# Performance work log

Measured on AMD Instinct MI355X. Metric: run time of the kernel, lower is better.

## Reference

```python
import jax, jax.numpy as jnp
import numpy as np

MIN_RET = 0.1
TCI = 0.99
LN_EPS = 1e-6
BN_EPS = 1e-3


def _ln(x, g, b):
    m = x.mean(-1, keepdims=True)
    v = x.var(-1, keepdims=True)
    return (x - m) * jax.lax.rsqrt(v + LN_EPS) * g + b


def _mha(x, wq, bq, wk, bk, wv, bv, wo, bo):
    # keras MultiHeadAttention, inference (dropout off). Returns (out, weights[B,H,Tq,Tk]).
    dk = wq.shape[-1]
    q = jnp.einsum('bsd,dhk->bshk', x, wq) + bq
    k = jnp.einsum('bsd,dhk->bshk', x, wk) + bk
    v = jnp.einsum('bsd,dhk->bshk', x, wv) + bv
    s = jnp.einsum('bqhk,bshk->bhqs', q, k) * (1.0 / np.sqrt(dk))
    w = jax.nn.softmax(s, axis=-1)
    o = jnp.einsum('bhqs,bshk->bqhk', w, v)
    return jnp.einsum('bqhk,hkd->bqd', o, wo) + bo, w


def _trunk(x, ln1_g, ln1_b, ln2_g, ln2_b, ln3_g, ln3_b,
           gq_w, gq_b, gk_w, gk_b, gv_w, gv_b, go_w, go_b,
           lq_w, lq_b, lk_w, lk_b, lv_w, lv_b, lo_w, lo_b,
           ffn_w1, ffn_b1, ffn_w2, ffn_b2):
    norm1 = _ln(x, ln1_g, ln1_b)
    a, aw = _mha(norm1, gq_w, gq_b, gk_w, gk_b, gv_w, gv_b, go_w, go_b)
    out1 = x + a
    norm2 = _ln(out1, ln2_g, ln2_b)
    la, law = _mha(norm2, lq_w, lq_b, lk_w, lk_b, lv_w, lv_b, lo_w, lo_b)
    out2 = out1 + la
    norm3 = _ln(out2, ln3_g, ln3_b)
    f = jnp.maximum(norm3 @ ffn_w1 + ffn_b1, 0.0) @ ffn_w2 + ffn_b2
    return out2 + f, aw, law


def _topk_indices(aw, law, seq_len):
    # importance: mean over heads then over query dim -> [B, Tk]
    imp = 0.7 * aw.mean(axis=(1, 2)) + 0.3 * law.mean(axis=(1, 2))
    imp = imp / (imp.sum(-1, keepdims=True) + 1e-10)
    sv, si = jax.lax.top_k(imp, imp.shape[-1])
    cum = jnp.cumsum(sv, axis=-1)
    num = (cum <= TCI).sum(-1)
    min_pts = int(round(seq_len * MIN_RET))
    num = jnp.minimum(jnp.maximum(num, min_pts), seq_len)
    # padded-to-common-k version of the per-sample ragged stack in the original
    k = int(jnp.max(num))
    return jnp.sort(si[:, :k], axis=-1)


def reference(x, ln1_g, ln1_b, ln2_g, ln2_b, ln3_g, ln3_b,
              gq_w, gq_b, gk_w, gk_b, gv_w, gv_b, go_w, go_b,
              lq_w, lq_b, lk_w, lk_b, lv_w, lv_b, lo_w, lo_b,
              ffn_w1, ffn_b1, ffn_w2, ffn_b2,
              res_w, res_b, bn_g, bn_b, bn_mean, bn_var):
    out3, aw, law = _trunk(x, ln1_g, ln1_b, ln2_g, ln2_b, ln3_g, ln3_b,
                           gq_w, gq_b, gk_w, gk_b, gv_w, gv_b, go_w, go_b,
                           lq_w, lq_b, lk_w, lk_b, lv_w, lv_b, lo_w, lo_b,
                           ffn_w1, ffn_b1, ffn_w2, ffn_b2)
    idx = _topk_indices(aw, law, x.shape[1])  # [B, K]
    gather = lambda t: jnp.take_along_axis(t, idx[..., None], axis=1)
    down = gather(out3) + gather(x @ res_w + res_b)
    # BatchNorm, inference mode (moving stats)
    down = (down - bn_mean) * jax.lax.rsqrt(bn_var + BN_EPS) * bn_g + bn_b
    return down, idx


def setup_inputs() -> dict:
    B, S, D, H, F = 4, 2048, 256, 8, 1024
    dk = D // H
    ks = iter(jax.random.split(jax.random.key(0), 32))
    w = lambda *sh: jax.random.normal(next(ks), sh, jnp.float32) * 0.02
    inp = {'x': jax.random.normal(next(ks), (B, S, D), jnp.float32)}
    for nm in ('ln1', 'ln2', 'ln3'):
        inp[nm + '_g'] = jnp.ones((D,), jnp.float32)
        inp[nm + '_b'] = jnp.zeros((D,), jnp.float32)
    for p in ('g', 'l'):
        for t in ('q', 'k', 'v'):
            inp[f'{p}{t}_w'] = w(D, H, dk)
            inp[f'{p}{t}_b'] = jnp.zeros((H, dk), jnp.float32)
        inp[f'{p}o_w'] = w(H, dk, D)
        inp[f'{p}o_b'] = jnp.zeros((D,), jnp.float32)
    inp['ffn_w1'] = w(D, F); inp['ffn_b1'] = jnp.zeros((F,), jnp.float32)
    inp['ffn_w2'] = w(F, D); inp['ffn_b2'] = jnp.zeros((D,), jnp.float32)
    inp['res_w'] = w(D, D); inp['res_b'] = jnp.zeros((D,), jnp.float32)
    inp['bn_g'] = jnp.ones((D,), jnp.float32)
    inp['bn_b'] = jnp.zeros((D,), jnp.float32)
    inp['bn_mean'] = jnp.zeros((D,), jnp.float32)
    inp['bn_var'] = jnp.ones((D,), jnp.float32)
    return inp
```

## Files before the change

### kernel.cpp

```cpp
#include <hip/hip_runtime.h>

#define SEQ 2048
#define DM 256
#define NH 8
#define DKH 32
#define NBATCH 4
#define QSCALE (0.17677669529663687f * 1.4426950408889634f)

#if __has_builtin(__builtin_amdgcn_exp2f)
#define EXP2(x) __builtin_amdgcn_exp2f(x)
#else
#define EXP2(x) exp2f(x)
#endif

typedef __attribute__((ext_vector_type(8))) __bf16 bf16x8;
typedef __attribute__((ext_vector_type(4))) float floatx4;
typedef __attribute__((ext_vector_type(8))) short short8v;
typedef __attribute__((ext_vector_type(2))) unsigned int uint2v;

__device__ inline unsigned short f2bf(float x){
  union { float f; unsigned u; } v; v.f = x;
  unsigned r = v.u + 0x7FFFu + ((v.u >> 16) & 1u);
  return (unsigned short)(r >> 16);
}
__device__ inline unsigned pack2bf(float a, float b){
  union { float f; unsigned u; } ua, ub; ua.f = a; ub.f = b;
  return __builtin_amdgcn_perm(ub.u, ua.u, 0x07060302u);
}

__global__ __launch_bounds__(256) void ln_kernel(const float* __restrict__ X,
    const float* __restrict__ G, const float* __restrict__ Bv,
    unsigned short* __restrict__ Y){
  int row = blockIdx.x*4 + (threadIdx.x>>6);
  int lane = threadIdx.x & 63;
  const float4 v = *(const float4*)(X + (size_t)row*DM + lane*4);
  float s = v.x+v.y+v.z+v.w;
  #pragma unroll
  for (int off=32; off; off>>=1) s += __shfl_xor(s, off, 64);
  float mean = s * (1.0f/DM);
  float dx=v.x-mean, dy=v.y-mean, dz=v.z-mean, dw=v.w-mean;
  float ss = dx*dx+dy*dy+dz*dz+dw*dw;
  #pragma unroll
  for (int off=32; off; off>>=1) ss += __shfl_xor(ss, off, 64);
  float r = rsqrtf(ss*(1.0f/DM) + 1e-6f);
  const float4 g = *(const float4*)(G + lane*4);
  const float4 b = *(const float4*)(Bv + lane*4);
  ushort4 o;
  o.x = f2bf(dx*r*g.x + b.x);
  o.y = f2bf(dy*r*g.y + b.y);
  o.z = f2bf(dz*r*g.z + b.z);
  o.w = f2bf(dw*r*g.w + b.w);
  *(ushort4*)(Y + (size_t)row*DM + lane*4) = o;
}

struct WtArgs {
  const float* src[12];
  unsigned short* dst[12];
  int K[12], N[12], stride[12], off[12];
  int blk0[13];
};
__global__ __launch_bounds__(256) void wtrans_all(WtArgs a){
  __shared__ unsigned short sT[64][40];
  int wi = 0;
  while (blockIdx.x >= (unsigned)a.blk0[wi+1]) ++wi;
  int blk = blockIdx.x - a.blk0[wi];
  int tid = threadIdx.x;
  if (wi == 11){
    const float* X = a.src[11];
    unsigned short* D = a.dst[11];
    int row = blk*8 + (tid>>5);
    int c8 = (tid & 31)*8;
    const float* ip = X + (size_t)row*256 + c8;
    float4 v0 = *(const float4*)ip, v1 = *(const float4*)(ip+4);
    union { short8v v; unsigned short u[8]; } pk;
    pk.u[0]=f2bf(v0.x); pk.u[1]=f2bf(v0.y); pk.u[2]=f2bf(v0.z); pk.u[3]=f2bf(v0.w);
    pk.u[4]=f2bf(v1.x); pk.u[5]=f2bf(v1.y); pk.u[6]=f2bf(v1.z); pk.u[7]=f2bf(v1.w);
    *(short8v*)(D + (size_t)row*1280 + 1024 + c8) = pk.v;
    return;
  }
  const float* W = a.src[wi];
  unsigned short* Wt = a.dst[wi];
  int K = a.K[wi], N = a.N[wi], stride = a.stride[wi], off = a.off[wi];
  int nbk = N >> 6;
  int bx = blk % nbk, by = blk / nbk;
  int k0 = by << 5, n0 = bx << 6;
  int r = tid >> 3, cs = (tid & 7) << 3;
  const float* ip = W + (size_t)(k0+r)*N + n0 + cs;
  float4 av = *(const float4*)ip;
  float4 bq = *(const float4*)(ip+4);
  sT[cs+0][r]=f2bf(av.x); sT[cs+1][r]=f2bf(av.y); sT[cs+2][r]=f2bf(av.z); sT[cs+3][r]=f2bf(av.w);
  sT[cs+4][r]=f2bf(bq.x); sT[cs+5][r]=f2bf(bq.y); sT[cs+6][r]=f2bf(bq.z); sT[cs+7][r]=f2bf(bq.w);
  __syncthreads();
  int n = tid >> 2, kc = (tid & 3) << 3;
  *(short8v*)(Wt + (size_t)(n0+n)*stride + off + k0 + kc) = *(const short8v*)(&sT[n][kc]);
}

__global__ __launch_bounds__(256) void gemm_bf16(const unsigned short* __restrict__ A,
    const unsigned short* __restrict__ Bt, const float* __restrict__ bias,
    const float* __restrict__ Res, void* __restrict__ Cout,
    int M, int N, int K, int flags, float outscale, int ldc){
  __shared__ unsigned short sA[8192];
  __shared__ unsigned short sB[4096];
  int nbk = N >> 6;
  int bx = blockIdx.x % nbk, by = blockIdx.x / nbk;
  int m0 = by << 7, n0 = bx << 6;
  int tid = threadIdx.x, w = tid >> 6, lane = tid & 63;
  int m16 = lane & 15, quad = lane >> 4;
  int wr = w & 1, wc = w >> 1;
  const unsigned short* pa[4]; const unsigned short* pb[2];
  #pragma unroll
  for (int i=0;i<4;++i){
    int c = tid + i*256;
    int l = c & 63, kk = (c>>6)&1, mt = c>>7;
    pa[i] = A + (size_t)(m0 + mt*16 + (l&15))*K + kk*32 + ((l>>4)<<3);
  }
  #pragma unroll
  for (int i=0;i<2;++i){
    int c = tid + i*256;
    int l = c & 63, kk = (c>>6)&1, nt = c>>7;
    pb[i] = Bt + (size_t)(n0 + nt*16 + (l&15))*K + kk*32 + ((l>>4)<<3);
  }
  short8v ar[4], br[2];
  #pragma unroll
  for (int i=0;i<4;++i) ar[i] = *(const short8v*)pa[i];
  #pragma unroll
  for (int i=0;i<2;++i) br[i] = *(const short8v*)pb[i];
  floatx4 acc[4][2];
  #pragma unroll
  for (int i=0;i<4;++i){ acc[i][0]=(floatx4){0,0,0,0}; acc[i][1]=(floatx4){0,0,0,0}; }
  for (int k0=0; k0<K; k0+=64){
    __syncthreads();
    #pragma unroll
    for (int i=0;i<4;++i) *(short8v*)(sA + (tid+i*256)*8) = ar[i];
    #pragma unroll
    for (int i=0;i<2;++i) *(short8v*)(sB + (tid+i*256)*8) = br[i];
    __syncthreads();
    if (k0 + 64 < K){
      #pragma unroll
      for (int i=0;i<4;++i) ar[i] = *(const short8v*)(pa[i] + k0 + 64);
      #pragma unroll
      for (int i=0;i<2;++i) br[i] = *(const short8v*)(pb[i] + k0 + 64);
    }
    #pragma unroll
    for (int kk=0;kk<2;++kk){
      bf16x8 bf0 = *(const bf16x8*)(sB + (((wc*2+0)*2+kk)*64 + lane)*8);
      bf16x8 bf1 = *(const bf16x8*)(sB + (((wc*2+1)*2+kk)*64 + lane)*8);
      #pragma unroll
      for (int mt=0;mt<4;++mt){
        bf16x8 af = *(const bf16x8*)(sA + (((wr*4+mt)*2+kk)*64 + lane)*8);
        acc[mt][0] = __builtin_amdgcn_mfma_f32_16x16x32_bf16(af, bf0, acc[mt][0], 0,0,0);
        acc[mt][1] = __builtin_amdgcn_mfma_f32_16x16x32_bf16(af, bf1, acc[mt][1], 0,0,0);
      }
    }
  }
  float b0 = bias ? bias[n0 + wc*32 + m16]      : 0.0f;
  float b1 = bias ? bias[n0 + wc*32 + 16 + m16] : 0.0f;
  #pragma unroll
  for (int mt=0;mt<4;++mt){
    #pragma unroll
    for (int r=0;r<4;++r){
      size_t row = (size_t)m0 + wr*64 + mt*16 + quad*4 + r;
      int col0 = n0 + wc*32 + m16, col1 = col0 + 16;
      float v0 = acc[mt][0][r] + b0, v1 = acc[mt][1][r] + b1;
      if (Res){ v0 += Res[row*N + col0]; v1 += Res[row*N + col1]; }
      if (flags & 1){ v0 = fmaxf(v0, 0.0f); v1 = fmaxf(v1, 0.0f); }
      v0 *= outscale; v1 *= outscale;
      if (flags & 2){
        unsigned short* C = (unsigned short*)Cout;
        C[row*ldc + col0] = f2bf(v0); C[row*ldc + col1] = f2bf(v1);
      } else {
        float* C = (float*)Cout;
        C[row*ldc + col0] = v0; C[row*ldc + col1] = v1;
      }
    }
  }
}

__global__ __launch_bounds__(256) void gemm64(const unsigned short* __restrict__ A,
    const unsigned short* __restrict__ Bt, const float* __restrict__ bias,
    const float* __restrict__ bias2, const float* __restrict__ Res,
    void* __restrict__ Cout, int M, int N, int K, int flags, float outscale){
  __shared__ unsigned short sA[4096];
  __shared__ unsigned short sB[4096];
  int nbk = N >> 6;
  int bx = blockIdx.x % nbk, by = blockIdx.x / nbk;
  int m0 = by << 6, n0 = bx << 6;
  int tid = threadIdx.x, w = tid >> 6, lane = tid & 63;
  int m16 = lane & 15, quad = lane >> 4;
  int wr = w & 1, wc = w >> 1;
  const unsigned short* pa[2]; const unsigned short* pb[2];
  #pragma unroll
  for (int i=0;i<2;++i){
    int c = tid + i*256;
    int l = c & 63, kk = (c>>6)&1, mt = c>>7;
    int col = kk*32 + ((l>>4)<<3);
    pa[i] = A  + (size_t)(m0 + mt*16 + (l&15))*K + col;
    pb[i] = Bt + (size_t)(n0 + mt*16 + (l&15))*K + col;
  }
  short8v ar[2], br[2];
  #pragma unroll
  for (int i=0;i<2;++i){ ar[i] = *(const short8v*)pa[i]; br[i] = *(const short8v*)pb[i]; }
  floatx4 acc[2][2];
  acc[0][0]=(floatx4){0,0,0,0}; acc[0][1]=(floatx4){0,0,0,0};
  acc[1][0]=(floatx4){0,0,0,0}; acc[1][1]=(floatx4){0,0,0,0};
  for (int k0=0; k0<K; k0+=64){
    __syncthreads();
    #pragma unroll
    for (int i=0;i<2;++i){
      *(short8v*)(sA + (tid+i*256)*8) = ar[i];
      *(short8v*)(sB + (tid+i*256)*8) = br[i];
    }
    __syncthreads();
    if (k0 + 64 < K){
      #pragma unroll
      for (int i=0;i<2;++i){ ar[i] = *(const short8v*)(pa[i]+k0+64); br[i] = *(const short8v*)(pb[i]+k0+64); }
    }
    #pragma unroll
    for (int kk=0;kk<2;++kk){
      bf16x8 bf0 = *(const bf16x8*)(sB + (((wc*2+0)*2+kk)*64 + lane)*8);
      bf16x8 bf1 = *(const bf16x8*)(sB + (((wc*2+1)*2+kk)*64 + lane)*8);
      bf16x8 af0 = *(const bf16x8*)(sA + (((wr*2+0)*2+kk)*64 + lane)*8);
      bf16x8 af1 = *(const bf16x8*)(sA + (((wr*2+1)*2+kk)*64 + lane)*8);
      acc[0][0] = __builtin_amdgcn_mfma_f32_16x16x32_bf16(af0, bf0, acc[0][0], 0,0,0);
      acc[0][1] = __builtin_amdgcn_mfma_f32_16x16x32_bf16(af0, bf1, acc[0][1], 0,0,0);
      acc[1][0] = __builtin_amdgcn_mfma_f32_16x16x32_bf16(af1, bf0, acc[1][0], 0,0,0);
      acc[1][1] = __builtin_amdgcn_mfma_f32_16x16x32_bf16(af1, bf1, acc[1][1], 0,0,0);
    }
  }
  float b0 = bias ? bias[n0 + wc*32 + m16]      : 0.0f;
  float b1 = bias ? bias[n0 + wc*32 + 16 + m16] : 0.0f;
  if (bias2){ b0 += bias2[n0 + wc*32 + m16]; b1 += bias2[n0 + wc*32 + 16 + m16]; }
  #pragma unroll
  for (int mt=0;mt<2;++mt){
    #pragma unroll
    for (int r=0;r<4;++r){
      size_t row = (size_t)m0 + (wr*2+mt)*16 + quad*4 + r;
      int col0 = n0 + wc*32 + m16, col1 = col0 + 16;
      float v0 = acc[mt][0][r] + b0, v1 = acc[mt][1][r] + b1;
      if (Res){ v0 += Res[row*N + col0]; v1 += Res[row*N + col1]; }
      if (flags & 1){ v0 = fmaxf(v0, 0.0f); v1 = fmaxf(v1, 0.0f); }
      v0 *= outscale; v1 *= outscale;
      if (flags & 2){
        unsigned short* C = (unsigned short*)Cout;
        C[row*N + col0] = f2bf(v0); C[row*N + col1] = f2bf(v1);
      } else {
        float* C = (float*)Cout;
        C[row*N + col0] = v0; C[row*N + col1] = v1;
      }
    }
  }
}

__global__ __launch_bounds__(256) void gemm_qkv(const unsigned short* __restrict__ A,
    const unsigned short* __restrict__ Bt,
    const float* __restrict__ bq, const float* __restrict__ bk, const float* __restrict__ bv,
    unsigned short* __restrict__ outq, unsigned short* __restrict__ outk,
    unsigned short* __restrict__ outvt){
  __shared__ unsigned short sA[8192];
  __shared__ unsigned short sB[4096];
  int bx = blockIdx.x % 12, by = blockIdx.x / 12;
  int m0 = by << 7, n0 = bx << 6;
  int tid = threadIdx.x, w = tid >> 6, lane = tid & 63;
  int m16 = lane & 15, quad = lane >> 4;
  int wr = w & 1, wc = w >> 1;
  const unsigned short* pa[4]; const unsigned short* pb[2];
  #pragma unroll
  for (int i=0;i<4;++i){
    int c = tid + i*256;
    int l = c & 63, kk = (c>>6)&1, mt = c>>7;
    pa[i] = A + (size_t)(m0 + mt*16 + (l&15))*256 + kk*32 + ((l>>4)<<3);
  }
  #pragma unroll
  for (int i=0;i<2;++i){
    int c = tid + i*256;
    int l = c & 63, kk = (c>>6)&1, nt = c>>7;
    pb[i] = Bt + (size_t)(n0 + nt*16 + (l&15))*256 + kk*32 + ((l>>4)<<3);
  }
  short8v ar[4], br[2];
  #pragma unroll
  for (int i=0;i<4;++i) ar[i] = *(const short8v*)pa[i];
  #pragma unroll
  for (int i=0;i<2;++i) br[i] = *(const short8v*)pb[i];
  floatx4 acc[4][2];
  #pragma unroll
  for (int i=0;i<4;++i){ acc[i][0]=(floatx4){0,0,0,0}; acc[i][1]=(floatx4){0,0,0,0}; }
  for (int k0=0; k0<256; k0+=64){
    __syncthreads();
    #pragma unroll
    for (int i=0;i<4;++i) *(short8v*)(sA + (tid+i*256)*8) = ar[i];
    #pragma unroll
    for (int i=0;i<2;++i) *(short8v*)(sB + (tid+i*256)*8) = br[i];
    __syncthreads();
    if (k0 + 64 < 256){
      #pragma unroll
      for (int i=0;i<4;++i) ar[i] = *(const short8v*)(pa[i] + k0 + 64);
      #pragma unroll
      for (int i=0;i<2;++i) br[i] = *(const short8v*)(pb[i] + k0 + 64);
    }
    #pragma unroll
    for (int kk=0;kk<2;++kk){
      bf16x8 bf0 = *(const bf16x8*)(sB + (((wc*2+0)*2+kk)*64 + lane)*8);
      bf16x8 bf1 = *(const bf16x8*)(sB + (((wc*2+1)*2+kk)*64 + lane)*8);
      #pragma unroll
      for (int mt=0;mt<4;++mt){
        bf16x8 af = *(const bf16x8*)(sA + (((wr*4+mt)*2+kk)*64 + lane)*8);
        acc[mt][0] = __builtin_amdgcn_mfma_f32_16x16x32_bf16(af, bf0, acc[mt][0], 0,0,0);
        acc[mt][1] = __builtin_amdgcn_mfma_f32_16x16x32_bf16(af, bf1, acc[mt][1], 0,0,0);
      }
    }
  }
  int seg = n0 >> 8;
  int nb  = n0 & 255;
  const float* bias = (seg==0) ? bq : ((seg==1) ? bk : bv);
  float b0 = bias[nb + wc*32 + m16];
  float b1 = bias[nb + wc*32 + 16 + m16];
  if (seg == 2){
    int b = m0 >> 11;
    int t0 = (m0 & 2047) + wr*64 + quad*4;
    #pragma unroll
    for (int mt=0;mt<4;++mt){
      int t = t0 + mt*16;
      #pragma unroll
      for (int cc=0;cc<2;++cc){
        int col = nb + wc*32 + m16 + cc*16;
        float bb = cc ? b1 : b0;
        int hh = col >> 5, dd = col & 31;
        uint2v pk;
        pk.x = (unsigned)f2bf(acc[mt][cc][0]+bb) | ((unsigned)f2bf(acc[mt][cc][1]+bb) << 16);
        pk.y = (unsigned)f2bf(acc[mt][cc][2]+bb) | ((unsigned)f2bf(acc[mt][cc][3]+bb) << 16);
        *(uint2v*)(outvt + ((size_t)((b*8+hh)*32+dd))*SEQ + t) = pk;
      }
    }
  } else {
    unsigned short* C = (seg==0) ? outq : outk;
    float scale = (seg==0) ? QSCALE : 1.0f;
    #pragma unroll
    for (int mt=0;mt<4;++mt){
      #pragma unroll
      for (int r=0;r<4;++r){
        size_t row = (size_t)m0 + wr*64 + mt*16 + quad*4 + r;
        int col0 = nb + wc*32 + m16, col1 = col0 + 16;
        C[row*256 + col0] = f2bf((acc[mt][0][r] + b0)*scale);
        C[row*256 + col1] = f2bf((acc[mt][1][r] + b1)*scale);
      }
    }
  }
}

__global__ __launch_bounds__(256) void flash_kernel(
    const unsigned short* __restrict__ Qb, const unsigned short* __restrict__ Kb,
    const unsigned short* __restrict__ Vt, unsigned short* __restrict__ Obf,
    float* __restrict__ Lout){
  __shared__ unsigned short sK[4096];
  __shared__ unsigned short sV[4096];
  __shared__ unsigned short sP[4*16*136];
  int qb = blockIdx.x & 31, bh = blockIdx.x >> 5;
  int h = bh & 7, b = bh >> 3;
  int tid = threadIdx.x, w = tid >> 6, lane = tid & 63;
  int m16 = lane & 15, quad = lane >> 4;
  int qrow0 = qb*64 + w*16;
  bf16x8 qf = *(const bf16x8*)(Qb + (size_t)(b*SEQ + qrow0 + m16)*DM + h*DKH + quad*8);
  floatx4 o0 = {0,0,0,0}, o1 = {0,0,0,0};
  float l0 = 0.f;
  unsigned short* sPw = sP + w*2176;

  const unsigned short* kp[2]; const unsigned short* vp[2];
  #pragma unroll
  for (int i=0;i<2;++i){
    int c = tid + i*256, l = c & 63;
    int kt = c >> 6;
    kp[i] = Kb + (size_t)(b*SEQ + kt*16 + (l&15))*DM + h*DKH + ((l>>4)<<3);
    int nt = (c>>6)&1, ks = c>>7;
    vp[i] = Vt + (size_t)(bh*DKH + nt*16 + (l&15))*SEQ + ks*32 + ((l>>4)<<3);
  }
  short8v kr[2], vr[2];
  #pragma unroll
  for (int i=0;i<2;++i){ kr[i] = *(const short8v*)kp[i]; vr[i] = *(const short8v*)vp[i]; }

  for (int t0=0; t0<SEQ; t0+=128){
    __syncthreads();
    #pragma unroll
    for (int i=0;i<2;++i){
      *(short8v*)(sK + (tid+i*256)*8) = kr[i];
      *(short8v*)(sV + (tid+i*256)*8) = vr[i];
    }
    __syncthreads();
    if (t0 + 128 < SEQ){
      #pragma unroll
      for (int i=0;i<2;++i){
        kr[i] = *(const short8v*)(kp[i] + (size_t)(t0+128)*DM);
        vr[i] = *(const short8v*)(vp[i] + (t0+128));
      }
    }
    #pragma unroll
    for (int kt=0;kt<8;++kt){
      bf16x8 kf = *(const bf16x8*)(sK + (kt*64+lane)*8);
      floatx4 z = {0,0,0,0};
      floatx4 s = __builtin_amdgcn_mfma_f32_16x16x32_bf16(kf, qf, z, 0,0,0);
      float p0 = EXP2(s[0]), p1 = EXP2(s[1]), p2 = EXP2(s[2]), p3 = EXP2(s[3]);
      l0 += (p0+p1)+(p2+p3);
      uint2v pk; pk.x = pack2bf(p0,p1); pk.y = pack2bf(p2,p3);
      *(uint2v*)(sPw + m16*136 + kt*16 + quad*4) = pk;
    }
    #pragma unroll
    for (int ks=0;ks<4;++ks){
      bf16x8 pf  = *(const bf16x8*)(sPw + m16*136 + ks*32 + quad*8);
      bf16x8 vf0 = *(const bf16x8*)(sV + ((ks*2+0)*64+lane)*8);
      bf16x8 vf1 = *(const bf16x8*)(sV + ((ks*2+1)*64+lane)*8);
      o0 = __builtin_amdgcn_mfma_f32_16x16x32_bf16(pf, vf0, o0, 0,0,0);
      o1 = __builtin_amdgcn_mfma_f32_16x16x32_bf16(pf, vf1, o1, 0,0,0);
    }
  }
  l0 += __shfl_xor(l0, 16, 64);
  l0 += __shfl_xor(l0, 32, 64);
  float inv = 1.0f / l0;
  #pragma unroll
  for (int r=0;r<4;++r){
    float iv = __shfl(inv, quad*4 + r, 64);
    int q = qrow0 + quad*4 + r;
    size_t base = (size_t)(b*SEQ + q)*DM + h*DKH;
    Obf[base + m16]      = f2bf(o0[r]*iv);
    Obf[base + 16 + m16] = f2bf(o1[r]*iv);
    if (m16 == 0) Lout[(size_t)bh*SEQ + q] = iv;
  }
}

__global__ __launch_bounds__(128) void colsum_kernel(
    const unsigned short* __restrict__ Qb, const unsigned short* __restrict__ Kb,
    const float* __restrict__ Lv, float* __restrict__ col){
  __shared__ unsigned short sQ[2048];
  __shared__ float sL[64];
  int kc = blockIdx.x & 31;
  int rest = blockIdx.x >> 5;
  int bh = rest & 31;
  int half = rest >> 5;
  int h = bh & 7, b = bh >> 3;
  int tid = threadIdx.x, w = tid >> 6, lane = tid & 63;
  int m16 = lane & 15, quad = lane >> 4;
  int key0 = kc*64 + w*32;
  const unsigned short* kp = Kb + (size_t)(b*SEQ + key0 + m16)*DM + h*DKH + quad*8;
  bf16x8 kf0 = *(const bf16x8*)kp;
  bf16x8 kf1 = *(const bf16x8*)(kp + 16*DM);
  float acc0[4] = {0,0,0,0}, acc1[4] = {0,0,0,0};
  const unsigned short* qp[2];
  #pragma unroll
  for (int i=0;i<2;++i){
    int c = tid + i*128, l = c & 63, qt = c >> 6;
    qp[i] = Qb + (size_t)(b*SEQ + half*1024 + qt*16 + (l&15))*DM + h*DKH + ((l>>4)<<3);
  }
  short8v qr[2];
  #pragma unroll
  for (int i=0;i<2;++i) qr[i] = *(const short8v*)qp[i];
  float lr = (tid < 64) ? Lv[(size_t)bh*SEQ + half*1024 + tid] : 0.0f;
  for (int q0=0; q0<1024; q0+=64){
    __syncthreads();
    #pragma unroll
    for (int i=0;i<2;++i) *(short8v*)(sQ + (tid+i*128)*8) = qr[i];
    if (tid < 64) sL[tid] = lr;
    __syncthreads();
    if (q0 + 64 < 1024){
      #pragma unroll
      for (int i=0;i<2;++i) qr[i] = *(const short8v*)(qp[i] + (size_t)(q0+64)*DM);
      if (tid < 64) lr = Lv[(size_t)bh*SEQ + half*1024 + q0 + 64 + tid];
    }
    floatx4 z = {0,0,0,0};
    #pragma unroll
    for (int qt2=0;qt2<4;++qt2){
      bf16x8 qf = *(const bf16x8*)(sQ + (qt2*64+lane)*8);
      floatx4 t0 = __builtin_amdgcn_mfma_f32_16x16x32_bf16(kf0, qf, z, 0,0,0);
      floatx4 t1 = __builtin_amdgcn_mfma_f32_16x16x32_bf16(kf1, qf, z, 0,0,0);
      float lq = sL[qt2*16+m16];
      #pragma unroll
      for (int r=0;r<4;++r){ acc0[r] += EXP2(t0[r])*lq; acc1[r] += EXP2(t1[r])*lq; }
    }
  }
  #pragma unroll
  for (int r=0;r<4;++r){
    float v0 = acc0[r], v1 = acc1[r];
    v0 += __shfl_xor(v0, 1, 64); v0 += __shfl_xor(v0, 2, 64);
    v0 += __shfl_xor(v0, 4, 64); v0 += __shfl_xor(v0, 8, 64);
    v1 += __shfl_xor(v1, 1, 64); v1 += __shfl_xor(v1, 2, 64);
    v1 += __shfl_xor(v1, 4, 64); v1 += __shfl_xor(v1, 8, 64);
    if (m16 == 0){
      size_t base = (size_t)(half*32 + bh)*SEQ;
      col[base + key0 + quad*4 + r]      = v0;
      col[base + key0 + 16 + quad*4 + r] = v1;
    }
  }
}

__global__ __launch_bounds__(128) void imp_kernel(const float* __restrict__ colG,
    const float* __restrict__ colL, float* __restrict__ imp){
  int i = blockIdx.x*128 + threadIdx.x;
  int b = i >> 11, t = i & 2047;
  double sg = 0.0, sl = 0.0;
  for (int h=0; h<8; ++h){
    size_t i0 = (size_t)(b*8+h)*SEQ + t;
    size_t i1 = (size_t)(32 + b*8+h)*SEQ + t;
    sg += (double)colG[i0] + (double)colG[i1];
    sl += (double)colL[i0] + (double)colL[i1];
  }
  imp[i] = (float)(0.7*sg + 0.3*sl);
}

__global__ __launch_bounds__(256) void rank_part(const float* __restrict__ imp,
    int* __restrict__ rp){
  __shared__ float sj[256];
  int jc = blockIdx.x & 7;
  int ic = (blockIdx.x >> 3) & 7;
  int b  = blockIdx.x >> 6;
  int tid = threadIdx.x;
  sj[tid] = imp[b*2048 + jc*256 + tid];
  __syncthreads();
  int i = ic*256 + tid;
  float v = imp[b*2048 + i];
  int jbase = jc*256;
  int r = 0;
  #pragma unroll 4
  for (int j=0; j<256; j+=4){
    float4 vj = *(const float4*)&sj[j];
    r += (vj.x > v) || (vj.x == v && (jbase+j+0) < i);
    r += (vj.y > v) || (vj.y == v && (jbase+j+1) < i);
    r += (vj.z > v) || (vj.z == v && (jbase+j+2) < i);
    r += (vj.w > v) || (vj.w == v && (jbase+j+3) < i);
  }
  rp[(size_t)jc*8192 + b*2048 + i] = r;
}

__global__ __launch_bounds__(256) void compact_kernel(const int* __restrict__ rp,
    int KK, int* __restrict__ idxout){
  __shared__ int swave[4];
  int b = blockIdx.x;
  int tid = threadIdx.x, w = tid >> 6, lane = tid & 63;
  int base = tid*8;
  int f[8]; int c = 0;
  #pragma unroll
  for (int j=0;j<8;++j){
    int rr = 0;
    #pragma unroll
    for (int c2=0;c2<8;++c2) rr += rp[(size_t)c2*8192 + b*2048 + base + j];
    f[j] = (rr < KK) ? 1 : 0; c += f[j];
  }
  int pref = c;
  #pragma unroll
  for (int off=1; off<64; off<<=1){
    int t = __shfl_up(pref, off, 64);
    if (lane >= off) pref += t;
  }
  if (lane == 63) swave[w] = pref;
  __syncthreads();
  int wbase = 0;
  for (int k=0;k<w;++k) wbase += swave[k];
  int pos = wbase + pref - c;
  #pragma unroll
  for (int j=0;j<8;++j){
    if (f[j]) idxout[b*KK + pos++] = base + j;
  }
}

__global__ __launch_bounds__(256) void final_kernel(const float* __restrict__ rb,
    const int* __restrict__ idx, const float* __restrict__ g, const float* __restrict__ bt,
    const float* __restrict__ mean, const float* __restrict__ var,
    float* __restrict__ out, int KK){
  int row = blockIdx.x*4 + (threadIdx.x>>6);
  int lane = threadIdx.x & 63;
  int total = NBATCH*KK;
  if (row < total){
    int b = row / KK;
    int src = idx[row];
    float4 v  = *(const float4*)(rb + ((size_t)(b*SEQ+src))*DM + lane*4);
    float4 gm = *(const float4*)(mean + lane*4);
    float4 gv = *(const float4*)(var  + lane*4);
    float4 gg = *(const float4*)(g    + lane*4);
    float4 gb = *(const float4*)(bt   + lane*4);
    float4 o;
    o.x = (v.x-gm.x)*rsqrtf(gv.x+1e-3f)*gg.x + gb.x;
    o.y = (v.y-gm.y)*rsqrtf(gv.y+1e-3f)*gg.y + gb.y;
    o.z = (v.z-gm.z)*rsqrtf(gv.z+1e-3f)*gg.z + gb.z;
    o.w = (v.w-gm.w)*rsqrtf(gv.w+1e-3f)*gg.w + gb.w;
    *(float4*)(out + (size_t)row*DM + lane*4) = o;
  }
  int gid = blockIdx.x*256 + threadIdx.x;
  if (gid < total) out[(size_t)total*DM + gid] = (float)idx[gid];
}

extern "C" void kernel_launch(void* const* d_in, const int* in_sizes, int n_in,
                              void* d_out, int out_size, void* d_ws, size_t ws_size,
                              hipStream_t stream){
  (void)in_sizes; (void)n_in; (void)ws_size;
  const float* x    = (const float*)d_in[0];
  const float* ln1g = (const float*)d_in[1];
  const float* ln1b = (const float*)d_in[2];
  const float* ln2g = (const float*)d_in[3];
  const float* ln2b = (const float*)d_in[4];
  const float* ln3g = (const float*)d_in[5];
  const float* ln3b = (const float*)d_in[6];
  const float* gqw = (const float*)d_in[7];  const float* gqb = (const float*)d_in[8];
  const float* gkw = (const float*)d_in[9];  const float* gkb = (const float*)d_in[10];
  const float* gvw = (const float*)d_in[11]; const float* gvb = (const float*)d_in[12];
  const float* gow = (const float*)d_in[13]; const float* gob = (const float*)d_in[14];
  const float* lqw = (const float*)d_in[15]; const float* lqb = (const float*)d_in[16];
  const float* lkw = (const float*)d_in[17]; const float* lkb = (const float*)d_in[18];
  const float* lvw = (const float*)d_in[19]; const float* lvb = (const float*)d_in[20];
  const float* low = (const float*)d_in[21]; const float* lob = (const float*)d_in[22];
  const float* fw1 = (const float*)d_in[23]; const float* fb1 = (const float*)d_in[24];
  const float* fw2 = (const float*)d_in[25]; const float* fb2 = (const float*)d_in[26];
  const float* resw = (const float*)d_in[27]; const float* resb = (const float*)d_in[28];
  const float* bng = (const float*)d_in[29]; const float* bnb = (const float*)d_in[30];
  const float* bnm = (const float*)d_in[31]; const float* bnv = (const float*)d_in[32];

  float* ws = (float*)d_ws;
  const size_t M1 = 2097152;
  float* r1 = ws;
  float* r2 = ws + M1;
  float* r3 = ws + 2*M1;
  unsigned short* nb  = (unsigned short*)(ws + 3*M1);
  unsigned short* qbf = (unsigned short*)(ws + 3*M1 + M1/2);
  unsigned short* kbf = (unsigned short*)(ws + 4*M1);
  unsigned short* vtb = (unsigned short*)(ws + 4*M1 + M1/2);
  unsigned short* obf = (unsigned short*)(ws + 5*M1);
  unsigned short* Acat = (unsigned short*)(ws + 6*M1);
  unsigned short* wT  = (unsigned short*)(ws + 9*M1);
  unsigned short* wgq = wT;            unsigned short* wgk = wT + 65536;
  unsigned short* wgv = wT + 131072;   unsigned short* wgo = wT + 196608;
  unsigned short* wlq = wT + 262144;   unsigned short* wlk = wT + 327680;
  unsigned short* wlv = wT + 393216;   unsigned short* wlo = wT + 458752;
  unsigned short* wf1  = wT + 524288;
  unsigned short* wcat = wT + 786432;
  float* Ls   = ws + 10*M1;
  float* colG = ws + 10*M1 + 65536;
  float* colL = ws + 10*M1 + 196608;
  float* impb = ws + 10*M1 + 327680;
  int*   rpb  = (int*)(ws + 10*M1 + 335872);
  int*   idxb = (int*)(ws + 10*M1 + 401408);

  int KK = out_size / (NBATCH*(DM+1));
  float* out = (float*)d_out;

  WtArgs wa;
  const float* srcs[12] = {gqw,gkw,gvw,gow,lqw,lkw,lvw,low, fw1, fw2, resw, x};
  unsigned short* dsts[12] = {wgq,wgk,wgv,wgo,wlq,wlk,wlv,wlo, wf1, wcat, wcat, Acat};
  int Ks[12]  = {256,256,256,256,256,256,256,256, 256, 1024, 256, 0};
  int Ns[12]  = {256,256,256,256,256,256,256,256, 1024, 256, 256, 0};
  int Ss[12]  = {256,256,256,256,256,256,256,256, 256, 1280, 1280, 0};
  int Os[12]  = {0,0,0,0,0,0,0,0, 0, 0, 1024, 0};
  int acc = 0;
  for (int i=0;i<12;++i){
    wa.src[i]=srcs[i]; wa.dst[i]=dsts[i]; wa.K[i]=Ks[i]; wa.N[i]=Ns[i];
    wa.stride[i]=Ss[i]; wa.off[i]=Os[i];
    wa.blk0[i]=acc;
    acc += (i==11) ? 1024 : (Ks[i]>>5)*(Ns[i]>>6);
  }
  wa.blk0[12]=acc;
  wtrans_all<<<acc,256,0,stream>>>(wa);

  ln_kernel<<<2048,256,0,stream>>>(x, ln1g, ln1b, nb);
  gemm_qkv<<<768,256,0,stream>>>(nb, wgq, gqb, gkb, gvb, qbf, kbf, vtb);
  flash_kernel<<<1024,256,0,stream>>>(qbf, kbf, vtb, obf, Ls);
  colsum_kernel<<<2048,128,0,stream>>>(qbf, kbf, Ls, colG);
  gemm64<<<512,256,0,stream>>>(obf, wgo, gob, nullptr, x, r1, 8192,256,256, 0, 1.0f);

  ln_kernel<<<2048,256,0,stream>>>(r1, ln2g, ln2b, nb);
  gemm_qkv<<<768,256,0,stream>>>(nb, wlq, lqb, lkb, lvb, qbf, kbf, vtb);
  flash_kernel<<<1024,256,0,stream>>>(qbf, kbf, vtb, obf, Ls);
  colsum_kernel<<<2048,128,0,stream>>>(qbf, kbf, Ls, colL);
  gemm64<<<512,256,0,stream>>>(obf, wlo, lob, nullptr, r1, r2, 8192,256,256, 0, 1.0f);

  ln_kernel<<<2048,256,0,stream>>>(r2, ln3g, ln3b, nb);
  gemm_bf16<<<1024,256,0,stream>>>(nb, wf1, fb1, nullptr, Acat, 8192,1024,256, 1|2, 1.0f, 1280);
  gemm64<<<512,256,0,stream>>>(Acat, wcat, fb2, resb, r2, r3, 8192,256,1280, 0, 1.0f);

  imp_kernel<<<64,128,0,stream>>>(colG, colL, impb);
  rank_part<<<256,256,0,stream>>>(impb, rpb);
  compact_kernel<<<NBATCH,256,0,stream>>>(rpb, KK, idxb);
  int total = NBATCH*KK;
  final_kernel<<<(total+3)/4,256,0,stream>>>(r3, idxb, bng, bnb, bnm, bnv, out, KK);
}
```

Measured before the change: 361.5 us.

## Split flash attention over key halves and keep P in registers

Attention is now split across two key-range halves, doubling the block count. Each half writes unnormalized fp32 partial outputs and row sums, and a new reduce kernel combines them, normalizes, and writes the bf16 output and inverse sums. The V-transpose store now uses a permuted token order so the exponentiated scores can feed the PV MFMA straight from registers, which removes the per-wave shared-memory P buffer. In exchange it adds an extra kernel launch and an fp32 partial round-trip through global memory, and it raises the launch-bounds occupancy hint.

Measured after the change: 390.9 us. 8.1% more time.

```diff
diff --git a/kernel.cpp b/kernel.cpp
--- a/kernel.cpp
+++ b/kernel.cpp
@@ -319,7 +319,8 @@
     int t0 = (m0 & 2047) + wr*64 + quad*4;
     #pragma unroll
     for (int mt=0;mt<4;++mt){
-      int t = t0 + mt*16;
+      int tt = t0 + mt*16;
+      int tp = (tt & ~31) | (((tt>>2)&3)<<3) | (((tt>>4)&1)<<2);
       #pragma unroll
       for (int cc=0;cc<2;++cc){
         int col = nb + wc*32 + m16 + cc*16;
@@ -328,7 +329,7 @@
         uint2v pk;
         pk.x = (unsigned)f2bf(acc[mt][cc][0]+bb) | ((unsigned)f2bf(acc[mt][cc][1]+bb) << 16);
         pk.y = (unsigned)f2bf(acc[mt][cc][2]+bb) | ((unsigned)f2bf(acc[mt][cc][3]+bb) << 16);
-        *(uint2v*)(outvt + ((size_t)((b*8+hh)*32+dd))*SEQ + t) = pk;
+        *(uint2v*)(outvt + ((size_t)((b*8+hh)*32+dd))*SEQ + tp) = pk;
       }
     }
   } else {
@@ -347,14 +348,15 @@
   }
 }
 
-__global__ __launch_bounds__(256) void flash_kernel(
+__global__ __launch_bounds__(256, 8) void flash_kernel(
     const unsigned short* __restrict__ Qb, const unsigned short* __restrict__ Kb,
-    const unsigned short* __restrict__ Vt, unsigned short* __restrict__ Obf,
-    float* __restrict__ Lout){
+    const unsigned short* __restrict__ Vt, float* __restrict__ opart,
+    float* __restrict__ lpart){
   __shared__ unsigned short sK[4096];
   __shared__ unsigned short sV[4096];
-  __shared__ unsigned short sP[4*16*136];
-  int qb = blockIdx.x & 31, bh = blockIdx.x >> 5;
+  int qb = blockIdx.x & 31;
+  int bh = (blockIdx.x >> 5) & 31;
+  int half = blockIdx.x >> 10;
   int h = bh & 7, b = bh >> 3;
   int tid = threadIdx.x, w = tid >> 6, lane = tid & 63;
   int m16 = lane & 15, quad = lane >> 4;
@@ -362,7 +364,7 @@
   bf16x8 qf = *(const bf16x8*)(Qb + (size_t)(b*SEQ + qrow0 + m16)*DM + h*DKH + quad*8);
   floatx4 o0 = {0,0,0,0}, o1 = {0,0,0,0};
   float l0 = 0.f;
-  unsigned short* sPw = sP + w*2176;
+  int tbeg = half*1024;
 
   const unsigned short* kp[2]; const unsigned short* vp[2];
   #pragma unroll
@@ -375,9 +377,12 @@
   }
   short8v kr[2], vr[2];
   #pragma unroll
-  for (int i=0;i<2;++i){ kr[i] = *(const short8v*)kp[i]; vr[i] = *(const short8v*)vp[i]; }
-
-  for (int t0=0; t0<SEQ; t0+=128){
+  for (int i=0;i<2;++i){
+    kr[i] = *(const short8v*)(kp[i] + (size_t)tbeg*DM);
+    vr[i] = *(const short8v*)(vp[i] + tbeg);
+  }
+
+  for (int t0=tbeg; t0<tbeg+1024; t0+=128){
     __syncthreads();
     #pragma unroll
     for (int i=0;i<2;++i){
@@ -385,7 +390,7 @@
       *(short8v*)(sV + (tid+i*256)*8) = vr[i];
     }
     __syncthreads();
-    if (t0 + 128 < SEQ){
+    if (t0 + 128 < tbeg + 1024){
       #pragma unroll
       for (int i=0;i<2;++i){
         kr[i] = *(const short8v*)(kp[i] + (size_t)(t0+128)*DM);
@@ -393,36 +398,55 @@
       }
     }
     #pragma unroll
-    for (int kt=0;kt<8;++kt){
-      bf16x8 kf = *(const bf16x8*)(sK + (kt*64+lane)*8);
+    for (int ks=0;ks<4;++ks){
+      bf16x8 kf0 = *(const bf16x8*)(sK + ((ks*2+0)*64+lane)*8);
+      bf16x8 kf1 = *(const bf16x8*)(sK + ((ks*2+1)*64+lane)*8);
       floatx4 z = {0,0,0,0};
-      floatx4 s = __builtin_amdgcn_mfma_f32_16x16x32_bf16(kf, qf, z, 0,0,0);
-      float p0 = EXP2(s[0]), p1 = EXP2(s[1]), p2 = EXP2(s[2]), p3 = EXP2(s[3]);
-      l0 += (p0+p1)+(p2+p3);
-      uint2v pk; pk.x = pack2bf(p0,p1); pk.y = pack2bf(p2,p3);
-      *(uint2v*)(sPw + m16*136 + kt*16 + quad*4) = pk;
-    }
-    #pragma unroll
-    for (int ks=0;ks<4;++ks){
-      bf16x8 pf  = *(const bf16x8*)(sPw + m16*136 + ks*32 + quad*8);
+      floatx4 s0 = __builtin_amdgcn_mfma_f32_16x16x32_bf16(kf0, qf, z, 0,0,0);
+      floatx4 s1 = __builtin_amdgcn_mfma_f32_16x16x32_bf16(kf1, qf, z, 0,0,0);
+      float p0 = EXP2(s0[0]), p1 = EXP2(s0[1]), p2 = EXP2(s0[2]), p3 = EXP2(s0[3]);
+      float p4 = EXP2(s1[0]), p5 = EXP2(s1[1]), p6 = EXP2(s1[2]), p7 = EXP2(s1[3]);
+      l0 += ((p0+p1)+(p2+p3)) + ((p4+p5)+(p6+p7));
+      union { bf16x8 v; unsigned u[4]; } pf;
+      pf.u[0] = pack2bf(p0,p1); pf.u[1] = pack2bf(p2,p3);
+      pf.u[2] = pack2bf(p4,p5); pf.u[3] = pack2bf(p6,p7);
       bf16x8 vf0 = *(const bf16x8*)(sV + ((ks*2+0)*64+lane)*8);
       bf16x8 vf1 = *(const bf16x8*)(sV + ((ks*2+1)*64+lane)*8);
-      o0 = __builtin_amdgcn_mfma_f32_16x16x32_bf16(pf, vf0, o0, 0,0,0);
-      o1 = __builtin_amdgcn_mfma_f32_16x16x32_bf16(pf, vf1, o1, 0,0,0);
+      o0 = __builtin_amdgcn_mfma_f32_16x16x32_bf16(pf.v, vf0, o0, 0,0,0);
+      o1 = __builtin_amdgcn_mfma_f32_16x16x32_bf16(pf.v, vf1, o1, 0,0,0);
     }
   }
   l0 += __shfl_xor(l0, 16, 64);
   l0 += __shfl_xor(l0, 32, 64);
-  float inv = 1.0f / l0;
+  if (quad == 0)
+    lpart[(size_t)half*65536 + bh*2048 + qrow0 + m16] = l0;
   #pragma unroll
   for (int r=0;r<4;++r){
-    float iv = __shfl(inv, quad*4 + r, 64);
     int q = qrow0 + quad*4 + r;
-    size_t base = (size_t)(b*SEQ + q)*DM + h*DKH;
-    Obf[base + m16]      = f2bf(o0[r]*iv);
-    Obf[base + 16 + m16] = f2bf(o1[r]*iv);
-    if (m16 == 0) Lout[(size_t)bh*SEQ + q] = iv;
-  }
+    size_t ob = ((size_t)(half*32 + bh)*2048 + q)*32;
+    opart[ob + m16]      = o0[r];
+    opart[ob + 16 + m16] = o1[r];
+  }
+}
+
+__global__ __launch_bounds__(256) void reduce_o(const float* __restrict__ opart,
+    const float* __restrict__ lpart, unsigned short* __restrict__ Obf,
+    float* __restrict__ Linv){
+  int e4 = blockIdx.x*256 + threadIdx.x;
+  int e = e4*4;
+  int row = e >> 5;
+  int dk0 = e & 31;
+  float la = lpart[row], lb = lpart[65536 + row];
+  float inv = 1.0f / (la + lb);
+  float4 oa = *(const float4*)(opart + e);
+  float4 ob = *(const float4*)(opart + 2097152 + e);
+  int bh = row >> 11, q = row & 2047;
+  int b = bh >> 3, h = bh & 7;
+  ushort4 o;
+  o.x = f2bf((oa.x+ob.x)*inv); o.y = f2bf((oa.y+ob.y)*inv);
+  o.z = f2bf((oa.z+ob.z)*inv); o.w = f2bf((oa.w+ob.w)*inv);
+  *(ushort4*)(Obf + ((size_t)(b*SEQ+q))*DM + h*DKH + dk0) = o;
+  if (dk0 == 0) Linv[row] = inv;
 }
 
 __global__ __launch_bounds__(128) void colsum_kernel(
@@ -627,12 +651,14 @@
   unsigned short* wlv = wT + 393216;   unsigned short* wlo = wT + 458752;
   unsigned short* wf1  = wT + 524288;
   unsigned short* wcat = wT + 786432;
-  float* Ls   = ws + 10*M1;
-  float* colG = ws + 10*M1 + 65536;
-  float* colL = ws + 10*M1 + 196608;
-  float* impb = ws + 10*M1 + 327680;
-  int*   rpb  = (int*)(ws + 10*M1 + 335872);
-  int*   idxb = (int*)(ws + 10*M1 + 401408);
+  float* Ls    = ws + 10*M1;
+  float* lpart = ws + 10*M1 + 65536;
+  float* colG  = ws + 10*M1 + 196608;
+  float* colL  = ws + 10*M1 + 327680;
+  float* impb  = ws + 10*M1 + 458752;
+  int*   rpb   = (int*)(ws + 10*M1 + 466944);
+  int*   idxb  = (int*)(ws + 10*M1 + 532480);
+  float* opart = ws + 11*M1;
 
   int KK = out_size / (NBATCH*(DM+1));
   float* out = (float*)d_out;
@@ -656,13 +682,15 @@
 
   ln_kernel<<<2048,256,0,stream>>>(x, ln1g, ln1b, nb);
   gemm_qkv<<<768,256,0,stream>>>(nb, wgq, gqb, gkb, gvb, qbf, kbf, vtb);
-  flash_kernel<<<1024,256,0,stream>>>(qbf, kbf, vtb, obf, Ls);
+  flash_kernel<<<2048,256,0,stream>>>(qbf, kbf, vtb, opart, lpart);
+  reduce_o<<<2048,256,0,stream>>>(opart, lpart, obf, Ls);
   colsum_kernel<<<2048,128,0,stream>>>(qbf, kbf, Ls, colG);
   gemm64<<<512,256,0,stream>>>(obf, wgo, gob, nullptr, x, r1, 8192,256,256, 0, 1.0f);
 
   ln_kernel<<<2048,256,0,stream>>>(r1, ln2g, ln2b, nb);
   gemm_qkv<<<768,256,0,stream>>>(nb, wlq, lqb, lkb, lvb, qbf, kbf, vtb);
-  flash_kernel<<<1024,256,0,stream>>>(qbf, kbf, vtb, obf, Ls);
+  flash_kernel<<<2048,256,0,stream>>>(qbf, kbf, vtb, opart, lpart);
+  reduce_o<<<2048,256,0,stream>>>(opart, lpart, obf, Ls);
   colsum_kernel<<<2048,128,0,stream>>>(qbf, kbf, Ls, colL);
   gemm64<<<512,256,0,stream>>>(obf, wlo, lob, nullptr, r1, r2, 8192,256,256, 0, 1.0f);
 
```

## Keep softmax probabilities in registers by permuting V^T layout to match MFMA

Applied to the files above, without the earlier changes.

The V projection epilogue now writes V^T with a permuted token order within each 32-token group, so the S accumulator layout of two QK^T MFMAs lines up directly with the A-operand layout of the PV MFMA. The flash kernel then packs the exponentials into a bf16x8 register and feeds the PV MFMA directly, removing the per-wave LDS buffer for P and its write/read round trip. The cost is a more complex index mapping that must agree exactly with the K-side layout, plus some extra register pressure.

Measured after the change: 358.1 us (median of 2 runs). About the same (-0.9%).

```diff
diff --git a/kernel.cpp b/kernel.cpp
--- a/kernel.cpp
+++ b/kernel.cpp
@@ -319,7 +319,8 @@
     int t0 = (m0 & 2047) + wr*64 + quad*4;
     #pragma unroll
     for (int mt=0;mt<4;++mt){
-      int t = t0 + mt*16;
+      int tt = t0 + mt*16;
+      int tp = (tt & ~31) | (((tt>>2)&3)<<3) | (((tt>>4)&1)<<2);
       #pragma unroll
       for (int cc=0;cc<2;++cc){
         int col = nb + wc*32 + m16 + cc*16;
@@ -328,7 +329,7 @@
         uint2v pk;
         pk.x = (unsigned)f2bf(acc[mt][cc][0]+bb) | ((unsigned)f2bf(acc[mt][cc][1]+bb) << 16);
         pk.y = (unsigned)f2bf(acc[mt][cc][2]+bb) | ((unsigned)f2bf(acc[mt][cc][3]+bb) << 16);
-        *(uint2v*)(outvt + ((size_t)((b*8+hh)*32+dd))*SEQ + t) = pk;
+        *(uint2v*)(outvt + ((size_t)((b*8+hh)*32+dd))*SEQ + tp) = pk;
       }
     }
   } else {
@@ -353,7 +354,6 @@
     float* __restrict__ Lout){
   __shared__ unsigned short sK[4096];
   __shared__ unsigned short sV[4096];
-  __shared__ unsigned short sP[4*16*136];
   int qb = blockIdx.x & 31, bh = blockIdx.x >> 5;
   int h = bh & 7, b = bh >> 3;
   int tid = threadIdx.x, w = tid >> 6, lane = tid & 63;
@@ -362,7 +362,6 @@
   bf16x8 qf = *(const bf16x8*)(Qb + (size_t)(b*SEQ + qrow0 + m16)*DM + h*DKH + quad*8);
   floatx4 o0 = {0,0,0,0}, o1 = {0,0,0,0};
   float l0 = 0.f;
-  unsigned short* sPw = sP + w*2176;
 
   const unsigned short* kp[2]; const unsigned short* vp[2];
   #pragma unroll
@@ -393,22 +392,22 @@
       }
     }
     #pragma unroll
-    for (int kt=0;kt<8;++kt){
-      bf16x8 kf = *(const bf16x8*)(sK + (kt*64+lane)*8);
+    for (int ks=0;ks<4;++ks){
+      bf16x8 kf0 = *(const bf16x8*)(sK + ((ks*2+0)*64+lane)*8);
+      bf16x8 kf1 = *(const bf16x8*)(sK + ((ks*2+1)*64+lane)*8);
       floatx4 z = {0,0,0,0};
-      floatx4 s = __builtin_amdgcn_mfma_f32_16x16x32_bf16(kf, qf, z, 0,0,0);
-      float p0 = EXP2(s[0]), p1 = EXP2(s[1]), p2 = EXP2(s[2]), p3 = EXP2(s[3]);
-      l0 += (p0+p1)+(p2+p3);
-      uint2v pk; pk.x = pack2bf(p0,p1); pk.y = pack2bf(p2,p3);
-      *(uint2v*)(sPw + m16*136 + kt*16 + quad*4) = pk;
-    }
-    #pragma unroll
-    for (int ks=0;ks<4;++ks){
-      bf16x8 pf  = *(const bf16x8*)(sPw + m16*136 + ks*32 + quad*8);
+      floatx4 s0 = __builtin_amdgcn_mfma_f32_16x16x32_bf16(kf0, qf, z, 0,0,0);
+      floatx4 s1 = __builtin_amdgcn_mfma_f32_16x16x32_bf16(kf1, qf, z, 0,0,0);
+      float p0 = EXP2(s0[0]), p1 = EXP2(s0[1]), p2 = EXP2(s0[2]), p3 = EXP2(s0[3]);
+      float p4 = EXP2(s1[0]), p5 = EXP2(s1[1]), p6 = EXP2(s1[2]), p7 = EXP2(s1[3]);
+      l0 += ((p0+p1)+(p2+p3)) + ((p4+p5)+(p6+p7));
+      union { bf16x8 v; unsigned u[4]; } pf;
+      pf.u[0] = pack2bf(p0,p1); pf.u[1] = pack2bf(p2,p3);
+      pf.u[2] = pack2bf(p4,p5); pf.u[3] = pack2bf(p6,p7);
       bf16x8 vf0 = *(const bf16x8*)(sV + ((ks*2+0)*64+lane)*8);
       bf16x8 vf1 = *(const bf16x8*)(sV + ((ks*2+1)*64+lane)*8);
-      o0 = __builtin_amdgcn_mfma_f32_16x16x32_bf16(pf, vf0, o0, 0,0,0);
-      o1 = __builtin_amdgcn_mfma_f32_16x16x32_bf16(pf, vf1, o1, 0,0,0);
+      o0 = __builtin_amdgcn_mfma_f32_16x16x32_bf16(pf.v, vf0, o0, 0,0,0);
+      o1 = __builtin_amdgcn_mfma_f32_16x16x32_bf16(pf.v, vf1, o1, 0,0,0);
     }
   }
   l0 += __shfl_xor(l0, 16, 64);
@@ -627,12 +626,12 @@
   unsigned short* wlv = wT + 393216;   unsigned short* wlo = wT + 458752;
   unsigned short* wf1  = wT + 524288;
   unsigned short* wcat = wT + 786432;
-  float* Ls   = ws + 10*M1;
-  float* colG = ws + 10*M1 + 65536;
-  float* colL = ws + 10*M1 + 196608;
-  float* impb = ws + 10*M1 + 327680;
-  int*   rpb  = (int*)(ws + 10*M1 + 335872);
-  int*   idxb = (int*)(ws + 10*M1 + 401408);
+  float* Ls    = ws + 10*M1;
+  float* colG  = ws + 10*M1 + 65536;
+  float* colL  = ws + 10*M1 + 196608;
+  float* impb  = ws + 10*M1 + 327680;
+  int*   rpb   = (int*)(ws + 10*M1 + 335872);
+  int*   idxb  = (int*)(ws + 10*M1 + 401408);
 
   int KK = out_size / (NBATCH*(DM+1));
   float* out = (float*)d_out;
```
